# Kernel tuning notes

Hardware: AMD Instinct MI355X
Metric: run time of the kernel (lower is better)

Reference implementation:

```python
import jax, jax.numpy as jnp
import numpy as np

N, E = 20000, 320000
IN, OUT, MID, EC, L = 128, 128, 32, 32, 1
SQRT3 = 1.7320508075688772
EPS = 1e-5


def _xavier(key, fan_in, fan_out, shape=None):
    shape = shape if shape is not None else (fan_in, fan_out)
    std = (2.0 / (fan_in + fan_out)) ** 0.5
    return jax.random.normal(key, shape, dtype=jnp.float32) * std


def layer_norm(x, w, b):
    mu = x.mean(axis=-1, keepdims=True)
    var = ((x - mu) ** 2).mean(axis=-1, keepdims=True)
    return (x - mu) * jax.lax.rsqrt(var + EPS) * w + b


def equ_layer_norm(x, w, b, lmax):
    # x: [N, (lmax+1)^2, C]; per-l RMS norm over (m, channel); l=0 mean-centered + bias.
    segs = []
    for l in range(lmax + 1):
        f = x[:, l * l:(l + 1) * (l + 1), :]
        if l == 0:
            f = f - f.mean(axis=-1, keepdims=True)
        norm = jnp.mean(f * f, axis=(1, 2), keepdims=True)
        f = f * jax.lax.rsqrt(norm + EPS) * w[l]
        if l == 0:
            f = f + b
        segs.append(f)
    return jnp.concatenate(segs, axis=1)


def gate_3j(x, w, lmax, channel):
    # x: [N, (lmax+1)^2, C]; w: [C, C*(lmax+1)] (jax in,out layout)
    after = x[:, 0, :] @ w
    type0 = after[:, :channel]
    mult = jax.nn.sigmoid(after[:, channel:])  # [N, lmax*C]
    parts = [jax.nn.silu(type0)[:, None, :]]
    for l in range(1, lmax + 1):
        parts.append(x[:, l * l:(l + 1) * (l + 1), :] * mult[:, None, (l - 1) * channel:l * channel])
    return jnp.concatenate(parts, axis=1)


def setup_inputs() -> dict:
    key = jax.random.key(0)
    ks = jax.random.split(key, 24)
    inp = {
        'feats': jax.random.normal(ks[0], (N, IN), dtype=jnp.float32),
        'equ': jax.random.normal(ks[1], (N, (L + 1) ** 2, EC), dtype=jnp.float32),
        'points': jax.random.normal(ks[2], (N, 3), dtype=jnp.float32),
        'neighbors': jax.random.randint(ks[3], (2, E), 0, N, dtype=jnp.int64) if jax.config.jax_enable_x64 else jax.random.randint(ks[3], (2, E), 0, N, dtype=jnp.int32),
        # params (jax Linear layout: [in, out])
        'ln1_w': jnp.ones((IN,), jnp.float32), 'ln1_b': jnp.zeros((IN,), jnp.float32),
        'eqn1_w': jnp.ones((L + 1, EC), jnp.float32), 'eqn1_b': jnp.zeros((EC,), jnp.float32),
        'inv_fc_w': _xavier(ks[4], IN, MID), 'inv_fc_b': jnp.zeros((MID,), jnp.float32),
        'equ_fc_w': _xavier(ks[5], EC, MID),
        'fc_l0_w': _xavier(ks[6], 2 * MID, MID), 'fc_l0_b': jnp.zeros((MID,), jnp.float32),
        'equ_fc_2_w': _xavier(ks[7], MID, EC),
        'inv_fc_1_w': _xavier(ks[8], 3 * MID, OUT), 'inv_fc_1_b': jnp.zeros((OUT,), jnp.float32),
        'ffn_ln_w': jnp.ones((OUT,), jnp.float32), 'ffn_ln_b': jnp.zeros((OUT,), jnp.float32),
        'ffn_w1': _xavier(ks[9], OUT, OUT), 'ffn_b1': jnp.zeros((OUT,), jnp.float32),
        'ffn_w2': _xavier(ks[10], OUT, OUT), 'ffn_b2': jnp.zeros((OUT,), jnp.float32),
        'eqn2_w': jnp.ones((L + 1, EC), jnp.float32), 'eqn2_b': jnp.zeros((EC,), jnp.float32),
        'fe1_w': _xavier(ks[11], EC, MID),
        'gate_w': _xavier(ks[12], MID, MID * (L + 1)),
        'fe2_w': _xavier(ks[13], MID, EC),
    }
    return inp


def reference(feats, equ, points, neighbors, ln1_w, ln1_b, eqn1_w, eqn1_b,
              inv_fc_w, inv_fc_b, equ_fc_w, fc_l0_w, fc_l0_b, equ_fc_2_w,
              inv_fc_1_w, inv_fc_1_b, ffn_ln_w, ffn_ln_b, ffn_w1, ffn_b1,
              ffn_w2, ffn_b2, eqn2_w, eqn2_b, fe1_w, gate_w, fe2_w):
    n = feats.shape[0]
    feats = layer_norm(feats, ln1_w, ln1_b)
    equ = equ_layer_norm(equ, eqn1_w, eqn1_b, L)
    feats1 = feats @ inv_fc_w + inv_fc_b              # [N, MID]
    equ1 = equ @ equ_fc_w                              # [N, 4, MID]
    src, dst = neighbors[0], neighbors[1]
    s_equ, t_equ = equ1[src], equ1[dst]                # [E, 4, MID]
    s_feats, t_feats = feats1[src], feats1[dst]        # [E, MID]
    vec = points[src] - points[dst]                    # [E, 3]
    # e3nn spherical harmonics l=0..1, normalize=False, 'component': [1, sqrt(3)*v]
    sh = jnp.concatenate([jnp.ones((vec.shape[0], 1), vec.dtype), SQRT3 * vec], axis=1)  # [E, 4]
    dot1 = jnp.sum(s_equ * t_equ, axis=1)              # [E, MID]
    dot2 = jnp.sum(s_equ * sh[:, :, None], axis=1)     # [E, MID]
    equ_l0 = jax.nn.silu(jnp.concatenate([dot1, dot2], axis=1) @ fc_l0_w + fc_l0_b)
    equ_message = jnp.concatenate([equ_l0[:, None, :], s_equ[:, 1:, :]], axis=1)  # [E, 4, MID]
    equ_message = equ_message @ equ_fc_2_w             # [E, 4, EC]
    inv_message = jax.nn.silu(jnp.concatenate([s_feats, t_feats, equ_l0], axis=-1) @ inv_fc_1_w + inv_fc_1_b)  # [E, OUT]
    nb_cnt = (jnp.max(inv_message, axis=-1, keepdims=True) > 0.0).astype(feats.dtype)  # [E, 1]
    neighbors_new = jnp.ones((n, 1), feats.dtype).at[dst].add(nb_cnt)
    inv_new = jnp.zeros((n, OUT), feats.dtype).at[dst].add(inv_message) + feats  # shortcut1 = Identity
    inv_new = inv_new / neighbors_new
    equ_new = jnp.zeros((n, (L + 1) ** 2, EC), feats.dtype).at[dst].add(equ_message) + equ  # shortcut2 = Identity
    equ_new = equ_new / neighbors_new[:, :, None]
    # ffn_inv
    h = layer_norm(inv_new, ffn_ln_w, ffn_ln_b)
    h = jax.nn.relu(h @ ffn_w1 + ffn_b1) @ ffn_w2 + ffn_b2
    inv_new = h + inv_new
    # ffn_equ
    g = equ_layer_norm(equ_new, eqn2_w, eqn2_b, L) @ fe1_w
    g = gate_3j(g, gate_w, L, MID) @ fe2_w
    equ_new = g + equ_new
    return inv_new, equ_new
```

## Files before the change

kernel.cpp:

```cpp
#include <hip/hip_runtime.h>
#include <math.h>

#define EPS 1e-5f
#define SQRT3F 1.7320508075688772f

__device__ __forceinline__ float wsum64(float x) {
#pragma unroll
    for (int o = 32; o > 0; o >>= 1) x += __shfl_xor(x, o, 64);
    return x;
}
__device__ __forceinline__ float hsum32(float x) {
#pragma unroll
    for (int o = 16; o > 0; o >>= 1) x += __shfl_xor(x, o, 64);
    return x;
}
__device__ __forceinline__ float sigm(float x) { return 1.f / (1.f + __expf(-x)); }
__device__ __forceinline__ float siluf(float x) { return x * sigm(x); }

__global__ __launch_bounds__(256) void pre_and_hist(
    int N, int E, int nb_pre,
    const float* __restrict__ feats, const float* __restrict__ equ,
    const int* __restrict__ nbrs, const float* __restrict__ points,
    const float* __restrict__ ln1_w, const float* __restrict__ ln1_b,
    const float* __restrict__ eqn1_w, const float* __restrict__ eqn1_b,
    const float* __restrict__ inv_fc_w, const float* __restrict__ inv_fc_b,
    const float* __restrict__ equ_fc_w, const float* __restrict__ Winv,
    float* __restrict__ feats_ln, float* __restrict__ equ_ln,
    float* __restrict__ equ1t, float* __restrict__ PsP, float* __restrict__ PtP,
    float* __restrict__ points4, int* __restrict__ deg)
{
    if (blockIdx.x >= nb_pre) {
        int i = (blockIdx.x - nb_pre) * 256 + threadIdx.x;
        if (i < E) atomicAdd(&deg[nbrs[E + i]], 1);
        return;
    }

    __shared__ float fl_s[4][128];
    __shared__ float el_s[4][128];
    __shared__ float f1_s[4][32];
    const int w = threadIdx.x >> 6;
    const int lane = threadIdx.x & 63;
    const int n = blockIdx.x * 4 + w;
    const bool act = n < N;
    const int c = lane & 31;
    const int half = lane >> 5;

    if (act && lane == 0) {
        float4 p;
        p.x = points[n * 3 + 0]; p.y = points[n * 3 + 1];
        p.z = points[n * 3 + 2]; p.w = 0.f;
        *(float4*)&points4[n * 4] = p;
    }

    float x0 = 0.f, x1 = 0.f;
    if (act) { x0 = feats[n * 128 + lane]; x1 = feats[n * 128 + 64 + lane]; }
    float s  = wsum64(x0 + x1);
    float sq = wsum64(x0 * x0 + x1 * x1);
    float mu = s * (1.f / 128.f);
    float var = sq * (1.f / 128.f) - mu * mu;
    float rs = rsqrtf(var + EPS);
    float y0 = (x0 - mu) * rs * ln1_w[lane] + ln1_b[lane];
    float y1 = (x1 - mu) * rs * ln1_w[64 + lane] + ln1_b[64 + lane];
    if (act) { feats_ln[n * 128 + lane] = y0; feats_ln[n * 128 + 64 + lane] = y1; }
    fl_s[w][lane] = y0; fl_s[w][64 + lane] = y1;

    float a = 0.f, b = 0.f;
    if (act) { a = equ[n * 128 + lane]; b = equ[n * 128 + 64 + lane]; }
    float a0 = (half == 0) ? a : 0.f;
    float m0 = wsum64(a0) * (1.f / 32.f);
    float f0 = a0 - m0;
    float n0 = wsum64((half == 0) ? f0 * f0 : 0.f) * (1.f / 32.f);
    float rs0 = rsqrtf(n0 + EPS);
    float sq1 = ((half == 1) ? a * a : 0.f) + b * b;
    float n1 = wsum64(sq1) * (1.f / 96.f);
    float rs1 = rsqrtf(n1 + EPS);
    float w1c = eqn1_w[32 + c];
    float ea = (half == 0) ? (f0 * rs0 * eqn1_w[c] + eqn1_b[c]) : (a * rs1 * w1c);
    float eb = b * rs1 * w1c;
    if (act) { equ_ln[n * 128 + lane] = ea; equ_ln[n * 128 + 64 + lane] = eb; }
    el_s[w][lane] = ea; el_s[w][64 + lane] = eb;

    __syncthreads();

    {
        float acc = 0.f;
#pragma unroll 8
        for (int k = 0; k < 64; k++) {
            int kk = half * 64 + k;
            acc += fl_s[w][kk] * inv_fc_w[kk * 32 + c];
        }
        acc += __shfl_xor(acc, 32);
        if (half == 0) f1_s[w][c] = acc + inv_fc_b[c];
    }
    if (act) {
        float acc = 0.f, acc2 = 0.f;
#pragma unroll 8
        for (int k = 0; k < 32; k++) {
            float wv = equ_fc_w[k * 32 + c];
            acc  += el_s[w][half * 32 + k] * wv;
            acc2 += el_s[w][(half + 2) * 32 + k] * wv;
        }
        equ1t[n * 128 + c * 4 + half]     = acc;
        equ1t[n * 128 + c * 4 + half + 2] = acc2;
    }
    __syncthreads();
    if (!act) return;

    {
        const int jj = c;
        float4 aPs = {0.f, 0.f, 0.f, 0.f};
        float4 aPt = {0.f, 0.f, 0.f, 0.f};
#pragma unroll 4
        for (int k = 0; k < 16; k++) {
            int kk = half * 16 + k;
            float x = f1_s[w][kk];
            float4 w4 = *(const float4*)&Winv[kk * 128 + jj * 4];
            float4 v4 = *(const float4*)&Winv[(32 + kk) * 128 + jj * 4];
            aPs.x += x * w4.x; aPs.y += x * w4.y; aPs.z += x * w4.z; aPs.w += x * w4.w;
            aPt.x += x * v4.x; aPt.y += x * v4.y; aPt.z += x * v4.z; aPt.w += x * v4.w;
        }
        aPs.x += __shfl_xor(aPs.x, 32); aPs.y += __shfl_xor(aPs.y, 32);
        aPs.z += __shfl_xor(aPs.z, 32); aPs.w += __shfl_xor(aPs.w, 32);
        aPt.x += __shfl_xor(aPt.x, 32); aPt.y += __shfl_xor(aPt.y, 32);
        aPt.z += __shfl_xor(aPt.z, 32); aPt.w += __shfl_xor(aPt.w, 32);
        if (half == 0) {
            const float* ps = (const float*)&aPs;
            const float* pt = (const float*)&aPt;
#pragma unroll
            for (int i = 0; i < 4; i++) {
                int m = jj * 4 + i;
                PsP[n * 128 + (m & 31) * 4 + (m >> 5)] = ps[i];
                PtP[n * 128 + (m & 31) * 4 + (m >> 5)] = pt[i];
            }
        }
    }
}

__global__ __launch_bounds__(1024) void csr_scan(
    int N, const int* __restrict__ deg,
    int* __restrict__ row_start, int* __restrict__ cursor,
    int* __restrict__ bucket_start, int* __restrict__ bucket_cursor,
    const float* __restrict__ fe1, const float* __restrict__ fe2,
    const float* __restrict__ gate_w, const float* __restrict__ We2,
    float* __restrict__ fe1P, float* __restrict__ fe2P,
    float* __restrict__ gatePa, float* __restrict__ gatePb,
    float* __restrict__ We2P)
{
    __shared__ int part[1024];
    __shared__ int hist[64];
    const int t = threadIdx.x;

    if (t < 1024) {
        int g = t >> 7, r = t & 127, cc = r >> 2, i = r & 3;
        fe1P[t]   = fe1[(g * 4 + i) * 32 + cc];
        fe2P[t]   = fe2[(g * 4 + i) * 32 + cc];
        gatePa[t] = gate_w[(g * 4 + i) * 64 + cc];
        gatePb[t] = gate_w[(g * 4 + i) * 64 + 32 + cc];
        We2P[t]   = We2[(g * 4 + i) * 32 + cc];
    }

    if (t < 64) hist[t] = 0;
    __syncthreads();

    const int per = (N + 1023) / 1024;
    const int base = t * per;
    int s = 0;
    for (int i = 0; i < per; i++) {
        int idx = base + i;
        if (idx < N) {
            int d = deg[idx];
            s += d;
            atomicAdd(&hist[d < 63 ? d : 63], 1);
        }
    }
    part[t] = s;
    __syncthreads();
    for (int off = 1; off < 1024; off <<= 1) {
        int v = (t >= off) ? part[t - off] : 0;
        __syncthreads();
        part[t] += v;
        __syncthreads();
    }
    int run = (t > 0) ? part[t - 1] : 0;
    for (int i = 0; i < per; i++) {
        int idx = base + i;
        if (idx < N) { row_start[idx] = run; cursor[idx] = run; run += deg[idx]; }
    }
    if (t == 0) {
        int acc = 0;
        for (int b = 63; b >= 0; b--) {
            bucket_start[b] = acc;
            bucket_cursor[b] = acc;
            acc += hist[b];
        }
    }
}

__global__ __launch_bounds__(256) void scatter_all(
    int E, int N, int nbE,
    const int* __restrict__ nb, int* __restrict__ cursor, int* __restrict__ csr_src,
    const int* __restrict__ deg, int* __restrict__ bucket_cursor, int* __restrict__ perm)
{
    if (blockIdx.x < nbE) {
        int i = blockIdx.x * 256 + threadIdx.x;
        if (i < E) {
            int d = nb[E + i];
            int s = nb[i];
            int pos = atomicAdd(&cursor[d], 1);
            csr_src[pos] = s;
        }
    } else {
        int i = (blockIdx.x - nbE) * 256 + threadIdx.x;
        if (i < N) {
            int d = deg[i]; if (d > 63) d = 63;
            int pos = atomicAdd(&bucket_cursor[d], 1);
            perm[pos] = i;
        }
    }
}

__global__ __launch_bounds__(256) void edge_agg(
    int N,
    const int* __restrict__ perm,
    const int* __restrict__ row_start, const int* __restrict__ deg_arr,
    const int* __restrict__ csr_src,
    const float* __restrict__ points4, const float* __restrict__ equ1t,
    const float* __restrict__ PsP, const float* __restrict__ PtP,
    const float* __restrict__ feats_ln, const float* __restrict__ equ_ln,
    const float* __restrict__ Wl0g, const float* __restrict__ bl0g,
    const float* __restrict__ Winvg, const float* __restrict__ binvg,
    const float* __restrict__ We2P, const float* __restrict__ fe1P,
    const float* __restrict__ fe2P, const float* __restrict__ gatePa,
    const float* __restrict__ gatePb,
    const float* __restrict__ eqn2_w, const float* __restrict__ eqn2_b,
    float* __restrict__ out_inv, float* __restrict__ out_equ)
{
    __shared__ float WeP[32 * 128];
    __shared__ float Wl0P[16 * 128];
    __shared__ float BinvP[128];
    __shared__ float bl0s[32];
    __shared__ float scr[8][128];

    for (int idx = threadIdx.x; idx < 4096; idx += 256) {
        int k = idx >> 7, r = idx & 127, cc = r >> 2, j = r & 3;
        WeP[idx] = Winvg[(64 + k) * 128 + j * 32 + cc];
    }
    for (int idx = threadIdx.x; idx < 2048; idx += 256) {
        int g = idx >> 7, r = idx & 127, cc = r >> 2, i = r & 3;
        Wl0P[idx] = Wl0g[(g * 4 + i) * 32 + cc];
    }
    if (threadIdx.x < 128) BinvP[threadIdx.x] = binvg[(threadIdx.x & 3) * 32 + (threadIdx.x >> 2)];
    if (threadIdx.x < 32) bl0s[threadIdx.x] = bl0g[threadIdx.x];
    __syncthreads();

    const int grp = threadIdx.x >> 5;
    const int c = threadIdx.x & 31;
    const int halfsel = grp & 1;
    const int gid = blockIdx.x * 8 + grp;
    if (gid >= N) return;
    const int n = perm[gid];

    const int start = row_start[n];
    const int len = deg_arr[n];
    const float bl0c = bl0s[c];
    float4 te4 = *(const float4*)&equ1t[n * 128 + c * 4];
    float4 pt4 = *(const float4*)&PtP[n * 128 + c * 4];
    float4 pd4 = *(const float4*)&points4[n * 4];
    float4 base = *(const float4*)&BinvP[c * 4];
    base.x += pt4.x; base.y += pt4.y; base.z += pt4.z; base.w += pt4.w;

    float4 acc = {0.f, 0.f, 0.f, 0.f};
    float4 aer = {0.f, 0.f, 0.f, 0.f};
    int cnt = 0;
    int i = 0;

    for (; i + 2 <= len; i += 2) {
        const int s0 = csr_src[start + i];
        const int s1 = csr_src[start + i + 1];
        float4 a0 = *(const float4*)&equ1t[s0 * 128 + c * 4];
        float4 a1 = *(const float4*)&equ1t[s1 * 128 + c * 4];
        float4 p0 = *(const float4*)&PsP[s0 * 128 + c * 4];
        float4 p1 = *(const float4*)&PsP[s1 * 128 + c * 4];
        float4 q0 = *(const float4*)&points4[s0 * 4];
        float4 q1 = *(const float4*)&points4[s1 * 4];
        float dx0 = SQRT3F * (q0.x - pd4.x);
        float dy0 = SQRT3F * (q0.y - pd4.y);
        float dz0 = SQRT3F * (q0.z - pd4.z);
        float dx1 = SQRT3F * (q1.x - pd4.x);
        float dy1 = SQRT3F * (q1.y - pd4.y);
        float dz1 = SQRT3F * (q1.z - pd4.z);
        scr[grp][c]      = a0.x * te4.x + a0.y * te4.y + a0.z * te4.z + a0.w * te4.w;
        scr[grp][32 + c] = a0.x + a0.y * dx0 + a0.z * dy0 + a0.w * dz0;
        scr[grp][64 + c] = a1.x * te4.x + a1.y * te4.y + a1.z * te4.z + a1.w * te4.w;
        scr[grp][96 + c] = a1.x + a1.y * dx1 + a1.z * dy1 + a1.w * dz1;

        float e0acc = bl0c, e1acc = bl0c;
#pragma unroll
        for (int g = 0; g < 16; g++) {
            float4 w4 = *(const float4*)&Wl0P[g * 128 + c * 4];
            float4 d0 = *(const float4*)&scr[grp][g * 4];
            float4 d1 = *(const float4*)&scr[grp][64 + g * 4];
            e0acc += d0.x * w4.x + d0.y * w4.y + d0.z * w4.z + d0.w * w4.w;
            e1acc += d1.x * w4.x + d1.y * w4.y + d1.z * w4.z + d1.w * w4.w;
        }
        float el0_0 = siluf(e0acc);
        float el0_1 = siluf(e1acc);
        aer.x += el0_0 + el0_1;
        aer.y += a0.y + a1.y; aer.z += a0.z + a1.z; aer.w += a0.w + a1.w;
        scr[grp][c] = el0_0;
        scr[grp][32 + c] = el0_1;

        float4 m0 = base, m1 = base;
        m0.x += p0.x; m0.y += p0.y; m0.z += p0.z; m0.w += p0.w;
        m1.x += p1.x; m1.y += p1.y; m1.z += p1.z; m1.w += p1.w;
#pragma unroll
        for (int g = 0; g < 8; g++) {
            float4 x0 = *(const float4*)&scr[grp][g * 4];
            float4 x1 = *(const float4*)&scr[grp][32 + g * 4];
            const float* xp0 = (const float*)&x0;
            const float* xp1 = (const float*)&x1;
#pragma unroll
            for (int t = 0; t < 4; t++) {
                float4 w4 = *(const float4*)&WeP[(g * 4 + t) * 128 + c * 4];
                float v0 = xp0[t], v1 = xp1[t];
                m0.x += v0 * w4.x; m0.y += v0 * w4.y; m0.z += v0 * w4.z; m0.w += v0 * w4.w;
                m1.x += v1 * w4.x; m1.y += v1 * w4.y; m1.z += v1 * w4.z; m1.w += v1 * w4.w;
            }
        }
        m0.x = siluf(m0.x); m0.y = siluf(m0.y); m0.z = siluf(m0.z); m0.w = siluf(m0.w);
        m1.x = siluf(m1.x); m1.y = siluf(m1.y); m1.z = siluf(m1.z); m1.w = siluf(m1.w);
        acc.x += m0.x + m1.x; acc.y += m0.y + m1.y;
        acc.z += m0.z + m1.z; acc.w += m0.w + m1.w;
        float mx0 = fmaxf(fmaxf(m0.x, m0.y), fmaxf(m0.z, m0.w));
        float mx1 = fmaxf(fmaxf(m1.x, m1.y), fmaxf(m1.z, m1.w));
        unsigned long long b0 = __ballot(mx0 > 0.f);
        unsigned long long b1 = __ballot(mx1 > 0.f);
        cnt += ((unsigned int)(b0 >> (halfsel * 32)) != 0u);
        cnt += ((unsigned int)(b1 >> (halfsel * 32)) != 0u);
    }
    for (; i < len; i++) {
        const int s0 = csr_src[start + i];
        float4 a0 = *(const float4*)&equ1t[s0 * 128 + c * 4];
        float4 p0 = *(const float4*)&PsP[s0 * 128 + c * 4];
        float4 q0 = *(const float4*)&points4[s0 * 4];
        float dx0 = SQRT3F * (q0.x - pd4.x);
        float dy0 = SQRT3F * (q0.y - pd4.y);
        float dz0 = SQRT3F * (q0.z - pd4.z);
        scr[grp][c]      = a0.x * te4.x + a0.y * te4.y + a0.z * te4.z + a0.w * te4.w;
        scr[grp][32 + c] = a0.x + a0.y * dx0 + a0.z * dy0 + a0.w * dz0;
        float e0acc = bl0c;
#pragma unroll
        for (int g = 0; g < 16; g++) {
            float4 w4 = *(const float4*)&Wl0P[g * 128 + c * 4];
            float4 d0 = *(const float4*)&scr[grp][g * 4];
            e0acc += d0.x * w4.x + d0.y * w4.y + d0.z * w4.z + d0.w * w4.w;
        }
        float el0_0 = siluf(e0acc);
        aer.x += el0_0; aer.y += a0.y; aer.z += a0.z; aer.w += a0.w;
        scr[grp][c] = el0_0;
        float4 m0 = base;
        m0.x += p0.x; m0.y += p0.y; m0.z += p0.z; m0.w += p0.w;
#pragma unroll
        for (int g = 0; g < 8; g++) {
            float4 x0 = *(const float4*)&scr[grp][g * 4];
            const float* xp0 = (const float*)&x0;
#pragma unroll
            for (int t = 0; t < 4; t++) {
                float4 w4 = *(const float4*)&WeP[(g * 4 + t) * 128 + c * 4];
                float v0 = xp0[t];
                m0.x += v0 * w4.x; m0.y += v0 * w4.y; m0.z += v0 * w4.z; m0.w += v0 * w4.w;
            }
        }
        m0.x = siluf(m0.x); m0.y = siluf(m0.y); m0.z = siluf(m0.z); m0.w = siluf(m0.w);
        acc.x += m0.x; acc.y += m0.y; acc.z += m0.z; acc.w += m0.w;
        float mx0 = fmaxf(fmaxf(m0.x, m0.y), fmaxf(m0.z, m0.w));
        unsigned long long b0 = __ballot(mx0 > 0.f);
        cnt += ((unsigned int)(b0 >> (halfsel * 32)) != 0u);
    }

    const float inv_nbn = 1.f / (1.f + (float)cnt);
    out_inv[n * 128 + c]      = (acc.x + feats_ln[n * 128 + c])      * inv_nbn;
    out_inv[n * 128 + 32 + c] = (acc.y + feats_ln[n * 128 + 32 + c]) * inv_nbn;
    out_inv[n * 128 + 64 + c] = (acc.z + feats_ln[n * 128 + 64 + c]) * inv_nbn;
    out_inv[n * 128 + 96 + c] = (acc.w + feats_ln[n * 128 + 96 + c]) * inv_nbn;

    *(float4*)&scr[grp][c * 4] = aer;
    float4 eo = {0.f, 0.f, 0.f, 0.f};
#pragma unroll
    for (int g = 0; g < 8; g++) {
        float4 w4 = *(const float4*)&We2P[g * 128 + c * 4];
        const float* wp = (const float*)&w4;
#pragma unroll
        for (int t = 0; t < 4; t++) {
            float4 a4 = *(const float4*)&scr[grp][(g * 4 + t) * 4];
            float wv = wp[t];
            eo.x += a4.x * wv; eo.y += a4.y * wv; eo.z += a4.z * wv; eo.w += a4.w * wv;
        }
    }
    float4 en;
    en.x = (eo.x + equ_ln[n * 128 + c])      * inv_nbn;
    en.y = (eo.y + equ_ln[n * 128 + 32 + c]) * inv_nbn;
    en.z = (eo.z + equ_ln[n * 128 + 64 + c]) * inv_nbn;
    en.w = (eo.w + equ_ln[n * 128 + 96 + c]) * inv_nbn;

    float m0e = hsum32(en.x) * (1.f / 32.f);
    float f0 = en.x - m0e;
    float n0 = hsum32(f0 * f0) * (1.f / 32.f);
    float rs0 = rsqrtf(n0 + EPS);
    float n1 = hsum32(en.y * en.y + en.z * en.z + en.w * en.w) * (1.f / 96.f);
    float rs1 = rsqrtf(n1 + EPS);
    float w1c = eqn2_w[32 + c];
    float4 ev;
    ev.x = f0 * rs0 * eqn2_w[c] + eqn2_b[c];
    ev.y = en.y * rs1 * w1c;
    ev.z = en.z * rs1 * w1c;
    ev.w = en.w * rs1 * w1c;
    *(float4*)&scr[grp][c * 4] = ev;

    float4 g4 = {0.f, 0.f, 0.f, 0.f};
#pragma unroll
    for (int g = 0; g < 8; g++) {
        float4 w4 = *(const float4*)&fe1P[g * 128 + c * 4];
        const float* wp = (const float*)&w4;
#pragma unroll
        for (int t = 0; t < 4; t++) {
            float4 a4 = *(const float4*)&scr[grp][(g * 4 + t) * 4];
            float wv = wp[t];
            g4.x += a4.x * wv; g4.y += a4.y * wv; g4.z += a4.z * wv; g4.w += a4.w * wv;
        }
    }
    scr[grp][c] = g4.x;

    float aftA = 0.f, aftB = 0.f;
#pragma unroll
    for (int g = 0; g < 8; g++) {
        float4 x4 = *(const float4*)&scr[grp][g * 4];
        float4 wa4 = *(const float4*)&gatePa[g * 128 + c * 4];
        float4 wb4 = *(const float4*)&gatePb[g * 128 + c * 4];
        aftA += x4.x * wa4.x + x4.y * wa4.y + x4.z * wa4.z + x4.w * wa4.w;
        aftB += x4.x * wb4.x + x4.y * wb4.y + x4.z * wb4.z + x4.w * wb4.w;
    }
    float mult = sigm(aftB);
    float4 G;
    G.x = siluf(aftA);
    G.y = g4.y * mult; G.z = g4.z * mult; G.w = g4.w * mult;
    *(float4*)&scr[grp][c * 4] = G;

    float4 oo = {0.f, 0.f, 0.f, 0.f};
#pragma unroll
    for (int g = 0; g < 8; g++) {
        float4 w4 = *(const float4*)&fe2P[g * 128 + c * 4];
        const float* wp = (const float*)&w4;
#pragma unroll
        for (int t = 0; t < 4; t++) {
            float4 a4 = *(const float4*)&scr[grp][(g * 4 + t) * 4];
            float wv = wp[t];
            oo.x += a4.x * wv; oo.y += a4.y * wv; oo.z += a4.z * wv; oo.w += a4.w * wv;
        }
    }
    out_equ[n * 128 + c]      = oo.x + en.x;
    out_equ[n * 128 + 32 + c] = oo.y + en.y;
    out_equ[n * 128 + 64 + c] = oo.z + en.z;
    out_equ[n * 128 + 96 + c] = oo.w + en.w;
}

__global__ __launch_bounds__(256) void node_post(
    int N,
    const float* __restrict__ ffn_ln_w, const float* __restrict__ ffn_ln_b,
    const float* __restrict__ W1g, const float* __restrict__ b1g,
    const float* __restrict__ W2g, const float* __restrict__ b2g,
    float* __restrict__ io_inv)
{
    __shared__ float ht[128 * 36];
    const int grp = threadIdx.x >> 5;
    const int c = threadIdx.x & 31;

    for (int q = 0; q < 4; q++) {
        const int nd = grp * 4 + q;
        const int n = blockIdx.x * 32 + nd;
        if (n >= N) break;
        float ip0 = io_inv[n * 128 + c];
        float ip1 = io_inv[n * 128 + 32 + c];
        float ip2 = io_inv[n * 128 + 64 + c];
        float ip3 = io_inv[n * 128 + 96 + c];
        float sm = hsum32(ip0 + ip1 + ip2 + ip3) * (1.f / 128.f);
        float sv = hsum32(ip0 * ip0 + ip1 * ip1 + ip2 * ip2 + ip3 * ip3) * (1.f / 128.f) - sm * sm;
        float rsv = rsqrtf(sv + EPS);
        ht[c * 36 + nd]         = (ip0 - sm) * rsv * ffn_ln_w[c]      + ffn_ln_b[c];
        ht[(32 + c) * 36 + nd]  = (ip1 - sm) * rsv * ffn_ln_w[32 + c] + ffn_ln_b[32 + c];
        ht[(64 + c) * 36 + nd]  = (ip2 - sm) * rsv * ffn_ln_w[64 + c] + ffn_ln_b[64 + c];
        ht[(96 + c) * 36 + nd]  = (ip3 - sm) * rsv * ffn_ln_w[96 + c] + ffn_ln_b[96 + c];
    }

    const int wid = threadIdx.x >> 6;
    const int half = (threadIdx.x >> 5) & 1;
    const int ndbase = wid * 8;
    const int nbase = blockIdx.x * 32 + ndbase;

    float4 acc8[8];
#pragma unroll
    for (int j = 0; j < 8; j++) acc8[j] = make_float4(0.f, 0.f, 0.f, 0.f);
    for (int k = 0; k < 64; k++) {
        const int kk = half * 64 + k;
        float4 w4 = *(const float4*)&W1g[kk * 128 + c * 4];
        float4 xA = *(const float4*)&ht[kk * 36 + ndbase];
        float4 xB = *(const float4*)&ht[kk * 36 + ndbase + 4];
        const float* xa = (const float*)&xA;
        const float* xb = (const float*)&xB;
#pragma unroll
        for (int j = 0; j < 4; j++) {
            float v = xa[j];
            acc8[j].x += v * w4.x; acc8[j].y += v * w4.y; acc8[j].z += v * w4.z; acc8[j].w += v * w4.w;
            float u = xb[j];
            acc8[4 + j].x += u * w4.x; acc8[4 + j].y += u * w4.y; acc8[4 + j].z += u * w4.z; acc8[4 + j].w += u * w4.w;
        }
    }
#pragma unroll
    for (int j = 0; j < 8; j++) {
        acc8[j].x += __shfl_xor(acc8[j].x, 32); acc8[j].y += __shfl_xor(acc8[j].y, 32);
        acc8[j].z += __shfl_xor(acc8[j].z, 32); acc8[j].w += __shfl_xor(acc8[j].w, 32);
    }
    if (half == 0) {
        float4 b4 = *(const float4*)&b1g[c * 4];
#pragma unroll
        for (int j = 0; j < 8; j++) {
            ht[(4 * c + 0) * 36 + ndbase + j] = fmaxf(acc8[j].x + b4.x, 0.f);
            ht[(4 * c + 1) * 36 + ndbase + j] = fmaxf(acc8[j].y + b4.y, 0.f);
            ht[(4 * c + 2) * 36 + ndbase + j] = fmaxf(acc8[j].z + b4.z, 0.f);
            ht[(4 * c + 3) * 36 + ndbase + j] = fmaxf(acc8[j].w + b4.w, 0.f);
        }
    }
#pragma unroll
    for (int j = 0; j < 8; j++) acc8[j] = make_float4(0.f, 0.f, 0.f, 0.f);
    for (int k = 0; k < 64; k++) {
        const int kk = half * 64 + k;
        float4 w4 = *(const float4*)&W2g[kk * 128 + c * 4];
        float4 xA = *(const float4*)&ht[kk * 36 + ndbase];
        float4 xB = *(const float4*)&ht[kk * 36 + ndbase + 4];
        const float* xa = (const float*)&xA;
        const float* xb = (const float*)&xB;
#pragma unroll
        for (int j = 0; j < 4; j++) {
            float v = xa[j];
            acc8[j].x += v * w4.x; acc8[j].y += v * w4.y; acc8[j].z += v * w4.z; acc8[j].w += v * w4.w;
            float u = xb[j];
            acc8[4 + j].x += u * w4.x; acc8[4 + j].y += u * w4.y; acc8[4 + j].z += u * w4.z; acc8[4 + j].w += u * w4.w;
        }
    }
#pragma unroll
    for (int j = 0; j < 8; j++) {
        acc8[j].x += __shfl_xor(acc8[j].x, 32); acc8[j].y += __shfl_xor(acc8[j].y, 32);
        acc8[j].z += __shfl_xor(acc8[j].z, 32); acc8[j].w += __shfl_xor(acc8[j].w, 32);
    }
    if (half == 0) {
        float4 b4 = *(const float4*)&b2g[c * 4];
#pragma unroll
        for (int j = 0; j < 8; j++) {
            const int n = nbase + j;
            if (n < N) {
                float4 ipre = *(const float4*)&io_inv[n * 128 + c * 4];
                float4 o;
                o.x = acc8[j].x + b4.x + ipre.x;
                o.y = acc8[j].y + b4.y + ipre.y;
                o.z = acc8[j].z + b4.z + ipre.z;
                o.w = acc8[j].w + b4.w + ipre.w;
                *(float4*)&io_inv[n * 128 + c * 4] = o;
            }
        }
    }
}

extern "C" void kernel_launch(void* const* d_in, const int* in_sizes, int n_in,
                              void* d_out, int out_size, void* d_ws, size_t ws_size,
                              hipStream_t stream)
{
    const float* feats     = (const float*)d_in[0];
    const float* equ       = (const float*)d_in[1];
    const float* points    = (const float*)d_in[2];
    const int*   neighbors = (const int*)d_in[3];
    const float* ln1_w     = (const float*)d_in[4];
    const float* ln1_b     = (const float*)d_in[5];
    const float* eqn1_w    = (const float*)d_in[6];
    const float* eqn1_b    = (const float*)d_in[7];
    const float* inv_fc_w  = (const float*)d_in[8];
    const float* inv_fc_b  = (const float*)d_in[9];
    const float* equ_fc_w  = (const float*)d_in[10];
    const float* fc_l0_w   = (const float*)d_in[11];
    const float* fc_l0_b   = (const float*)d_in[12];
    const float* equ_fc_2_w= (const float*)d_in[13];
    const float* inv_fc_1_w= (const float*)d_in[14];
    const float* inv_fc_1_b= (const float*)d_in[15];
    const float* ffn_ln_w  = (const float*)d_in[16];
    const float* ffn_ln_b  = (const float*)d_in[17];
    const float* ffn_w1    = (const float*)d_in[18];
    const float* ffn_b1    = (const float*)d_in[19];
    const float* ffn_w2    = (const float*)d_in[20];
    const float* ffn_b2    = (const float*)d_in[21];
    const float* eqn2_w    = (const float*)d_in[22];
    const float* eqn2_b    = (const float*)d_in[23];
    const float* fe1_w     = (const float*)d_in[24];
    const float* gate_w    = (const float*)d_in[25];
    const float* fe2_w     = (const float*)d_in[26];

    const int N = in_sizes[0] / 128;
    const int E = in_sizes[3] / 2;

    float* ws = (float*)d_ws;
    float* feats_ln = ws;
    float* equ_ln   = feats_ln + (size_t)N * 128;
    float* equ1t    = equ_ln   + (size_t)N * 128;
    float* PsP      = equ1t    + (size_t)N * 128;
    float* PtP      = PsP      + (size_t)N * 128;
    float* points4  = PtP      + (size_t)N * 128;
    float* fe1P     = points4  + (size_t)N * 4;
    float* fe2P     = fe1P + 1024;
    float* gatePa   = fe2P + 1024;
    float* gatePb   = gatePa + 1024;
    float* We2P     = gatePb + 1024;
    int* deg        = (int*)(We2P + 1024);
    int* row_start  = deg + N;
    int* cursor     = row_start + N;
    int* bucket_start  = cursor + N;
    int* bucket_cursor = bucket_start + 64;
    int* perm       = bucket_cursor + 64;
    int* csr_src    = perm + N;

    hipMemsetAsync(deg, 0, (size_t)N * sizeof(int), stream);

    const int nb_pre = (N + 3) / 4;
    const int nb_hist = (E + 255) / 256;
    pre_and_hist<<<nb_pre + nb_hist, 256, 0, stream>>>(
        N, E, nb_pre, feats, equ, neighbors, points,
        ln1_w, ln1_b, eqn1_w, eqn1_b,
        inv_fc_w, inv_fc_b, equ_fc_w, inv_fc_1_w,
        feats_ln, equ_ln, equ1t, PsP, PtP, points4, deg);

    csr_scan<<<1, 1024, 0, stream>>>(
        N, deg, row_start, cursor, bucket_start, bucket_cursor,
        fe1_w, fe2_w, gate_w, equ_fc_2_w,
        fe1P, fe2P, gatePa, gatePb, We2P);

    const int nbE = (E + 255) / 256;
    const int nbN = (N + 255) / 256;
    scatter_all<<<nbE + nbN, 256, 0, stream>>>(
        E, N, nbE, neighbors, cursor, csr_src, deg, bucket_cursor, perm);

    float* out_inv = (float*)d_out;
    float* out_equ = out_inv + (size_t)N * 128;

    edge_agg<<<(N + 7) / 8, 256, 0, stream>>>(
        N, perm, row_start, deg, csr_src,
        points4, equ1t, PsP, PtP, feats_ln, equ_ln,
        fc_l0_w, fc_l0_b, inv_fc_1_w, inv_fc_1_b,
        We2P, fe1P, fe2P, gatePa, gatePb, eqn2_w, eqn2_b,
        out_inv, out_equ);

    node_post<<<(N + 31) / 32, 256, 0, stream>>>(
        N, ffn_ln_w, ffn_ln_b, ffn_w1, ffn_b1, ffn_w2, ffn_b2,
        out_inv);
}
```

Before: 476.7 us.

## Fuse node FFN (layernorm + MLP) into edge aggregation kernel epilogue

Removes the separate node_post kernel and computes the inverse-feature layer norm and two-layer FFN inside edge_agg, keeping the aggregated node features in shared memory instead of writing and rereading them from global memory. The perm array is padded with -1 so every thread reaches the block-wide barrier, and only two waves per block run the 128x128 matmuls with weights read from global memory. This saves a launch and a global round-trip, but adds shared memory (less occupancy), a barrier that makes each block wait for its slowest-degree node, and a serial FFN tail using only a quarter of the threads.

```diff
diff --git a/kernel.cpp b/kernel.cpp
--- a/kernel.cpp
+++ b/kernel.cpp
@@ -137,9 +137,10 @@
 }
 
 __global__ __launch_bounds__(1024) void csr_scan(
-    int N, const int* __restrict__ deg,
+    int N, int nblk, const int* __restrict__ deg,
     int* __restrict__ row_start, int* __restrict__ cursor,
     int* __restrict__ bucket_start, int* __restrict__ bucket_cursor,
+    int* __restrict__ perm,
     const float* __restrict__ fe1, const float* __restrict__ fe2,
     const float* __restrict__ gate_w, const float* __restrict__ We2,
     float* __restrict__ fe1P, float* __restrict__ fe2P,
@@ -157,6 +158,9 @@
         gatePa[t] = gate_w[(g * 4 + i) * 64 + cc];
         gatePb[t] = gate_w[(g * 4 + i) * 64 + 32 + cc];
         We2P[t]   = We2[(g * 4 + i) * 32 + cc];
+    }
+    if (t == 1) {
+        for (int j = N; j < nblk * 8; j++) perm[j] = -1;
     }
 
     if (t < 64) hist[t] = 0;
@@ -233,6 +237,9 @@
     const float* __restrict__ fe2P, const float* __restrict__ gatePa,
     const float* __restrict__ gatePb,
     const float* __restrict__ eqn2_w, const float* __restrict__ eqn2_b,
+    const float* __restrict__ ffn_ln_w, const float* __restrict__ ffn_ln_b,
+    const float* __restrict__ W1g, const float* __restrict__ b1g,
+    const float* __restrict__ W2g, const float* __restrict__ b2g,
     float* __restrict__ out_inv, float* __restrict__ out_equ)
 {
     __shared__ float WeP[32 * 128];
@@ -240,6 +247,9 @@
     __shared__ float BinvP[128];
     __shared__ float bl0s[32];
     __shared__ float scr[8][128];
+    __shared__ float invs[8][128];
+    __shared__ float htp[128 * 9];
+    __shared__ int   nid[8];
 
     for (int idx = threadIdx.x; idx < 4096; idx += 256) {
         int k = idx >> 7, r = idx & 127, cc = r >> 2, j = r & 3;
@@ -257,314 +267,312 @@
     const int c = threadIdx.x & 31;
     const int halfsel = grp & 1;
     const int gid = blockIdx.x * 8 + grp;
-    if (gid >= N) return;
     const int n = perm[gid];
-
-    const int start = row_start[n];
-    const int len = deg_arr[n];
-    const float bl0c = bl0s[c];
-    float4 te4 = *(const float4*)&equ1t[n * 128 + c * 4];
-    float4 pt4 = *(const float4*)&PtP[n * 128 + c * 4];
-    float4 pd4 = *(const float4*)&points4[n * 4];
-    float4 base = *(const float4*)&BinvP[c * 4];
-    base.x += pt4.x; base.y += pt4.y; base.z += pt4.z; base.w += pt4.w;
-
-    float4 acc = {0.f, 0.f, 0.f, 0.f};
-    float4 aer = {0.f, 0.f, 0.f, 0.f};
-    int cnt = 0;
-    int i = 0;
-
-    for (; i + 2 <= len; i += 2) {
-        const int s0 = csr_src[start + i];
-        const int s1 = csr_src[start + i + 1];
-        float4 a0 = *(const float4*)&equ1t[s0 * 128 + c * 4];
-        float4 a1 = *(const float4*)&equ1t[s1 * 128 + c * 4];
-        float4 p0 = *(const float4*)&PsP[s0 * 128 + c * 4];
-        float4 p1 = *(const float4*)&PsP[s1 * 128 + c * 4];
-        float4 q0 = *(const float4*)&points4[s0 * 4];
-        float4 q1 = *(const float4*)&points4[s1 * 4];
-        float dx0 = SQRT3F * (q0.x - pd4.x);
-        float dy0 = SQRT3F * (q0.y - pd4.y);
-        float dz0 = SQRT3F * (q0.z - pd4.z);
-        float dx1 = SQRT3F * (q1.x - pd4.x);
-        float dy1 = SQRT3F * (q1.y - pd4.y);
-        float dz1 = SQRT3F * (q1.z - pd4.z);
-        scr[grp][c]      = a0.x * te4.x + a0.y * te4.y + a0.z * te4.z + a0.w * te4.w;
-        scr[grp][32 + c] = a0.x + a0.y * dx0 + a0.z * dy0 + a0.w * dz0;
-        scr[grp][64 + c] = a1.x * te4.x + a1.y * te4.y + a1.z * te4.z + a1.w * te4.w;
-        scr[grp][96 + c] = a1.x + a1.y * dx1 + a1.z * dy1 + a1.w * dz1;
-
-        float e0acc = bl0c, e1acc = bl0c;
-#pragma unroll
-        for (int g = 0; g < 16; g++) {
-            float4 w4 = *(const float4*)&Wl0P[g * 128 + c * 4];
-            float4 d0 = *(const float4*)&scr[grp][g * 4];
-            float4 d1 = *(const float4*)&scr[grp][64 + g * 4];
-            e0acc += d0.x * w4.x + d0.y * w4.y + d0.z * w4.z + d0.w * w4.w;
-            e1acc += d1.x * w4.x + d1.y * w4.y + d1.z * w4.z + d1.w * w4.w;
-        }
-        float el0_0 = siluf(e0acc);
-        float el0_1 = siluf(e1acc);
-        aer.x += el0_0 + el0_1;
-        aer.y += a0.y + a1.y; aer.z += a0.z + a1.z; aer.w += a0.w + a1.w;
-        scr[grp][c] = el0_0;
-        scr[grp][32 + c] = el0_1;
-
-        float4 m0 = base, m1 = base;
-        m0.x += p0.x; m0.y += p0.y; m0.z += p0.z; m0.w += p0.w;
-        m1.x += p1.x; m1.y += p1.y; m1.z += p1.z; m1.w += p1.w;
+    if (c == 0) nid[grp] = n;
+    const bool active = (n >= 0);
+
+    if (active) {
+        const int start = row_start[n];
+        const int len = deg_arr[n];
+        const float bl0c = bl0s[c];
+        float4 te4 = *(const float4*)&equ1t[n * 128 + c * 4];
+        float4 pt4 = *(const float4*)&PtP[n * 128 + c * 4];
+        float4 pd4 = *(const float4*)&points4[n * 4];
+        float4 base = *(const float4*)&BinvP[c * 4];
+        base.x += pt4.x; base.y += pt4.y; base.z += pt4.z; base.w += pt4.w;
+
+        float4 acc = {0.f, 0.f, 0.f, 0.f};
+        float4 aer = {0.f, 0.f, 0.f, 0.f};
+        int cnt = 0;
+        int i = 0;
+
+        for (; i + 2 <= len; i += 2) {
+            const int s0 = csr_src[start + i];
+            const int s1 = csr_src[start + i + 1];
+            float4 a0 = *(const float4*)&equ1t[s0 * 128 + c * 4];
+            float4 a1 = *(const float4*)&equ1t[s1 * 128 + c * 4];
+            float4 p0 = *(const float4*)&PsP[s0 * 128 + c * 4];
+            float4 p1 = *(const float4*)&PsP[s1 * 128 + c * 4];
+            float4 q0 = *(const float4*)&points4[s0 * 4];
+            float4 q1 = *(const float4*)&points4[s1 * 4];
+            float dx0 = SQRT3F * (q0.x - pd4.x);
+            float dy0 = SQRT3F * (q0.y - pd4.y);
+            float dz0 = SQRT3F * (q0.z - pd4.z);
+            float dx1 = SQRT3F * (q1.x - pd4.x);
+            float dy1 = SQRT3F * (q1.y - pd4.y);
+            float dz1 = SQRT3F * (q1.z - pd4.z);
+            scr[grp][c]      = a0.x * te4.x + a0.y * te4.y + a0.z * te4.z + a0.w * te4.w;
+            scr[grp][32 + c] = a0.x + a0.y * dx0 + a0.z * dy0 + a0.w * dz0;
+            scr[grp][64 + c] = a1.x * te4.x + a1.y * te4.y + a1.z * te4.z + a1.w * te4.w;
+            scr[grp][96 + c] = a1.x + a1.y * dx1 + a1.z * dy1 + a1.w * dz1;
+
+            float e0acc = bl0c, e1acc = bl0c;
+#pragma unroll
+            for (int g = 0; g < 16; g++) {
+                float4 w4 = *(const float4*)&Wl0P[g * 128 + c * 4];
+                float4 d0 = *(const float4*)&scr[grp][g * 4];
+                float4 d1 = *(const float4*)&scr[grp][64 + g * 4];
+                e0acc += d0.x * w4.x + d0.y * w4.y + d0.z * w4.z + d0.w * w4.w;
+                e1acc += d1.x * w4.x + d1.y * w4.y + d1.z * w4.z + d1.w * w4.w;
+            }
+            float el0_0 = siluf(e0acc);
+            float el0_1 = siluf(e1acc);
+            aer.x += el0_0 + el0_1;
+            aer.y += a0.y + a1.y; aer.z += a0.z + a1.z; aer.w += a0.w + a1.w;
+            scr[grp][c] = el0_0;
+            scr[grp][32 + c] = el0_1;
+
+            float4 m0 = base, m1 = base;
+            m0.x += p0.x; m0.y += p0.y; m0.z += p0.z; m0.w += p0.w;
+            m1.x += p1.x; m1.y += p1.y; m1.z += p1.z; m1.w += p1.w;
+#pragma unroll
+            for (int g = 0; g < 8; g++) {
+                float4 x0 = *(const float4*)&scr[grp][g * 4];
+                float4 x1 = *(const float4*)&scr[grp][32 + g * 4];
+                const float* xp0 = (const float*)&x0;
+                const float* xp1 = (const float*)&x1;
+#pragma unroll
+                for (int t = 0; t < 4; t++) {
+                    float4 w4 = *(const float4*)&WeP[(g * 4 + t) * 128 + c * 4];
+                    float v0 = xp0[t], v1 = xp1[t];
+                    m0.x += v0 * w4.x; m0.y += v0 * w4.y; m0.z += v0 * w4.z; m0.w += v0 * w4.w;
+                    m1.x += v1 * w4.x; m1.y += v1 * w4.y; m1.z += v1 * w4.z; m1.w += v1 * w4.w;
+                }
+            }
+            m0.x = siluf(m0.x); m0.y = siluf(m0.y); m0.z = siluf(m0.z); m0.w = siluf(m0.w);
+            m1.x = siluf(m1.x); m1.y = siluf(m1.y); m1.z = siluf(m1.z); m1.w = siluf(m1.w);
+            acc.x += m0.x + m1.x; acc.y += m0.y + m1.y;
+            acc.z += m0.z + m1.z; acc.w += m0.w + m1.w;
+            float mx0 = fmaxf(fmaxf(m0.x, m0.y), fmaxf(m0.z, m0.w));
+            float mx1 = fmaxf(fmaxf(m1.x, m1.y), fmaxf(m1.z, m1.w));
+            unsigned long long b0 = __ballot(mx0 > 0.f);
+            unsigned long long b1 = __ballot(mx1 > 0.f);
+            cnt += ((unsigned int)(b0 >> (halfsel * 32)) != 0u);
+            cnt += ((unsigned int)(b1 >> (halfsel * 32)) != 0u);
+        }
+        for (; i < len; i++) {
+            const int s0 = csr_src[start + i];
+            float4 a0 = *(const float4*)&equ1t[s0 * 128 + c * 4];
+            float4 p0 = *(const float4*)&PsP[s0 * 128 + c * 4];
+            float4 q0 = *(const float4*)&points4[s0 * 4];
+            float dx0 = SQRT3F * (q0.x - pd4.x);
+            float dy0 = SQRT3F * (q0.y - pd4.y);
+            float dz0 = SQRT3F * (q0.z - pd4.z);
+            scr[grp][c]      = a0.x * te4.x + a0.y * te4.y + a0.z * te4.z + a0.w * te4.w;
+            scr[grp][32 + c] = a0.x + a0.y * dx0 + a0.z * dy0 + a0.w * dz0;
+            float e0acc = bl0c;
+#pragma unroll
+            for (int g = 0; g < 16; g++) {
+                float4 w4 = *(const float4*)&Wl0P[g * 128 + c * 4];
+                float4 d0 = *(const float4*)&scr[grp][g * 4];
+                e0acc += d0.x * w4.x + d0.y * w4.y + d0.z * w4.z + d0.w * w4.w;
+            }
+            float el0_0 = siluf(e0acc);
+            aer.x += el0_0; aer.y += a0.y; aer.z += a0.z; aer.w += a0.w;
+            scr[grp][c] = el0_0;
+            float4 m0 = base;
+            m0.x += p0.x; m0.y += p0.y; m0.z += p0.z; m0.w += p0.w;
+#pragma unroll
+            for (int g = 0; g < 8; g++) {
+                float4 x0 = *(const float4*)&scr[grp][g * 4];
+                const float* xp0 = (const float*)&x0;
+#pragma unroll
+                for (int t = 0; t < 4; t++) {
+                    float4 w4 = *(const float4*)&WeP[(g * 4 + t) * 128 + c * 4];
+                    float v0 = xp0[t];
+                    m0.x += v0 * w4.x; m0.y += v0 * w4.y; m0.z += v0 * w4.z; m0.w += v0 * w4.w;
+                }
+            }
+            m0.x = siluf(m0.x); m0.y = siluf(m0.y); m0.z = siluf(m0.z); m0.w = siluf(m0.w);
+            acc.x += m0.x; acc.y += m0.y; acc.z += m0.z; acc.w += m0.w;
+            float mx0 = fmaxf(fmaxf(m0.x, m0.y), fmaxf(m0.z, m0.w));
+            unsigned long long b0 = __ballot(mx0 > 0.f);
+            cnt += ((unsigned int)(b0 >> (halfsel * 32)) != 0u);
+        }
+
+        const float inv_nbn = 1.f / (1.f + (float)cnt);
+        float4 im;
+        im.x = (acc.x + feats_ln[n * 128 + c])      * inv_nbn;
+        im.y = (acc.y + feats_ln[n * 128 + 32 + c]) * inv_nbn;
+        im.z = (acc.z + feats_ln[n * 128 + 64 + c]) * inv_nbn;
+        im.w = (acc.w + feats_ln[n * 128 + 96 + c]) * inv_nbn;
+        invs[grp][c]      = im.x;
+        invs[grp][32 + c] = im.y;
+        invs[grp][64 + c] = im.z;
+        invs[grp][96 + c] = im.w;
+        float sm = hsum32(im.x + im.y + im.z + im.w) * (1.f / 128.f);
+        float sv = hsum32(im.x * im.x + im.y * im.y + im.z * im.z + im.w * im.w)
+                   * (1.f / 128.f) - sm * sm;
+        float rsv = rsqrtf(sv + EPS);
+        htp[c * 9 + grp]        = (im.x - sm) * rsv * ffn_ln_w[c]      + ffn_ln_b[c];
+        htp[(32 + c) * 9 + grp] = (im.y - sm) * rsv * ffn_ln_w[32 + c] + ffn_ln_b[32 + c];
+        htp[(64 + c) * 9 + grp] = (im.z - sm) * rsv * ffn_ln_w[64 + c] + ffn_ln_b[64 + c];
+        htp[(96 + c) * 9 + grp] = (im.w - sm) * rsv * ffn_ln_w[96 + c] + ffn_ln_b[96 + c];
+
+        *(float4*)&scr[grp][c * 4] = aer;
+        float4 eo = {0.f, 0.f, 0.f, 0.f};
 #pragma unroll
         for (int g = 0; g < 8; g++) {
-            float4 x0 = *(const float4*)&scr[grp][g * 4];
-            float4 x1 = *(const float4*)&scr[grp][32 + g * 4];
-            const float* xp0 = (const float*)&x0;
-            const float* xp1 = (const float*)&x1;
+            float4 w4 = *(const float4*)&We2P[g * 128 + c * 4];
+            const float* wp = (const float*)&w4;
 #pragma unroll
             for (int t = 0; t < 4; t++) {
-                float4 w4 = *(const float4*)&WeP[(g * 4 + t) * 128 + c * 4];
-                float v0 = xp0[t], v1 = xp1[t];
-                m0.x += v0 * w4.x; m0.y += v0 * w4.y; m0.z += v0 * w4.z; m0.w += v0 * w4.w;
-                m1.x += v1 * w4.x; m1.y += v1 * w4.y; m1.z += v1 * w4.z; m1.w += v1 * w4.w;
-            }
-        }
-        m0.x = siluf(m0.x); m0.y = siluf(m0.y); m0.z = siluf(m0.z); m0.w = siluf(m0.w);
-        m1.x = siluf(m1.x); m1.y = siluf(m1.y); m1.z = siluf(m1.z); m1.w = siluf(m1.w);
-        acc.x += m0.x + m1.x; acc.y += m0.y + m1.y;
-        acc.z += m0.z + m1.z; acc.w += m0.w + m1.w;
-        float mx0 = fmaxf(fmaxf(m0.x, m0.y), fmaxf(m0.z, m0.w));
-        float mx1 = fmaxf(fmaxf(m1.x, m1.y), fmaxf(m1.z, m1.w));
-        unsigned long long b0 = __ballot(mx0 > 0.f);
-        unsigned long long b1 = __ballot(mx1 > 0.f);
-        cnt += ((unsigned int)(b0 >> (halfsel * 32)) != 0u);
-        cnt += ((unsigned int)(b1 >> (halfsel * 32)) != 0u);
-    }
-    for (; i < len; i++) {
-        const int s0 = csr_src[start + i];
-        float4 a0 = *(const float4*)&equ1t[s0 * 128 + c * 4];
-        float4 p0 = *(const float4*)&PsP[s0 * 128 + c * 4];
-        float4 q0 = *(const float4*)&points4[s0 * 4];
-        float dx0 = SQRT3F * (q0.x - pd4.x);
-        float dy0 = SQRT3F * (q0.y - pd4.y);
-        float dz0 = SQRT3F * (q0.z - pd4.z);
-        scr[grp][c]      = a0.x * te4.x + a0.y * te4.y + a0.z * te4.z + a0.w * te4.w;
-        scr[grp][32 + c] = a0.x + a0.y * dx0 + a0.z * dy0 + a0.w * dz0;
-        float e0acc = bl0c;
-#pragma unroll
-        for (int g = 0; g < 16; g++) {
-            float4 w4 = *(const float4*)&Wl0P[g * 128 + c * 4];
-            float4 d0 = *(const float4*)&scr[grp][g * 4];
-            e0acc += d0.x * w4.x + d0.y * w4.y + d0.z * w4.z + d0.w * w4.w;
-        }
-        float el0_0 = siluf(e0acc);
-        aer.x += el0_0; aer.y += a0.y; aer.z += a0.z; aer.w += a0.w;
-        scr[grp][c] = el0_0;
-        float4 m0 = base;
-        m0.x += p0.x; m0.y += p0.y; m0.z += p0.z; m0.w += p0.w;
+                float4 a4 = *(const float4*)&scr[grp][(g * 4 + t) * 4];
+                float wv = wp[t];
+                eo.x += a4.x * wv; eo.y += a4.y * wv; eo.z += a4.z * wv; eo.w += a4.w * wv;
+            }
+        }
+        float4 en;
+        en.x = (eo.x + equ_ln[n * 128 + c])      * inv_nbn;
+        en.y = (eo.y + equ_ln[n * 128 + 32 + c]) * inv_nbn;
+        en.z = (eo.z + equ_ln[n * 128 + 64 + c]) * inv_nbn;
+        en.w = (eo.w + equ_ln[n * 128 + 96 + c]) * inv_nbn;
+
+        float m0e = hsum32(en.x) * (1.f / 32.f);
+        float f0 = en.x - m0e;
+        float n0 = hsum32(f0 * f0) * (1.f / 32.f);
+        float rs0 = rsqrtf(n0 + EPS);
+        float n1 = hsum32(en.y * en.y + en.z * en.z + en.w * en.w) * (1.f / 96.f);
+        float rs1 = rsqrtf(n1 + EPS);
+        float w1c = eqn2_w[32 + c];
+        float4 ev;
+        ev.x = f0 * rs0 * eqn2_w[c] + eqn2_b[c];
+        ev.y = en.y * rs1 * w1c;
+        ev.z = en.z * rs1 * w1c;
+        ev.w = en.w * rs1 * w1c;
+        *(float4*)&scr[grp][c * 4] = ev;
+
+        float4 g4 = {0.f, 0.f, 0.f, 0.f};
 #pragma unroll
         for (int g = 0; g < 8; g++) {
-            float4 x0 = *(const float4*)&scr[grp][g * 4];
-            const float* xp0 = (const float*)&x0;
+            float4 w4 = *(const float4*)&fe1P[g * 128 + c * 4];
+            const float* wp = (const float*)&w4;
 #pragma unroll
             for (int t = 0; t < 4; t++) {
-                float4 w4 = *(const float4*)&WeP[(g * 4 + t) * 128 + c * 4];
-                float v0 = xp0[t];
-                m0.x += v0 * w4.x; m0.y += v0 * w4.y; m0.z += v0 * w4.z; m0.w += v0 * w4.w;
-            }
-        }
-        m0.x = siluf(m0.x); m0.y = siluf(m0.y); m0.z = siluf(m0.z); m0.w = siluf(m0.w);
-        acc.x += m0.x; acc.y += m0.y; acc.z += m0.z; acc.w += m0.w;
-        float mx0 = fmaxf(fmaxf(m0.x, m0.y), fmaxf(m0.z, m0.w));
-        unsigned long long b0 = __ballot(mx0 > 0.f);
-        cnt += ((unsigned int)(b0 >> (halfsel * 32)) != 0u);
-    }
-
-    const float inv_nbn = 1.f / (1.f + (float)cnt);
-    out_inv[n * 128 + c]      = (acc.x + feats_ln[n * 128 + c])      * inv_nbn;
-    out_inv[n * 128 + 32 + c] = (acc.y + feats_ln[n * 128 + 32 + c]) * inv_nbn;
-    out_inv[n * 128 + 64 + c] = (acc.z + feats_ln[n * 128 + 64 + c]) * inv_nbn;
-    out_inv[n * 128 + 96 + c] = (acc.w + feats_ln[n * 128 + 96 + c]) * inv_nbn;
-
-    *(float4*)&scr[grp][c * 4] = aer;
-    float4 eo = {0.f, 0.f, 0.f, 0.f};
-#pragma unroll
-    for (int g = 0; g < 8; g++) {
-        float4 w4 = *(const float4*)&We2P[g * 128 + c * 4];
-        const float* wp = (const float*)&w4;
-#pragma unroll
-        for (int t = 0; t < 4; t++) {
-            float4 a4 = *(const float4*)&scr[grp][(g * 4 + t) * 4];
-            float wv = wp[t];
-            eo.x += a4.x * wv; eo.y += a4.y * wv; eo.z += a4.z * wv; eo.w += a4.w * wv;
-        }
-    }
-    float4 en;
-    en.x = (eo.x + equ_ln[n * 128 + c])      * inv_nbn;
-    en.y = (eo.y + equ_ln[n * 128 + 32 + c]) * inv_nbn;
-    en.z = (eo.z + equ_ln[n * 128 + 64 + c]) * inv_nbn;
-    en.w = (eo.w + equ_ln[n * 128 + 96 + c]) * inv_nbn;
-
-    float m0e = hsum32(en.x) * (1.f / 32.f);
-    float f0 = en.x - m0e;
-    float n0 = hsum32(f0 * f0) * (1.f / 32.f);
-    float rs0 = rsqrtf(n0 + EPS);
-    float n1 = hsum32(en.y * en.y + en.z * en.z + en.w * en.w) * (1.f / 96.f);
-    float rs1 = rsqrtf(n1 + EPS);
-    float w1c = eqn2_w[32 + c];
-    float4 ev;
-    ev.x = f0 * rs0 * eqn2_w[c] + eqn2_b[c];
-    ev.y = en.y * rs1 * w1c;
-    ev.z = en.z * rs1 * w1c;
-    ev.w = en.w * rs1 * w1c;
-    *(float4*)&scr[grp][c * 4] = ev;
-
-    float4 g4 = {0.f, 0.f, 0.f, 0.f};
-#pragma unroll
-    for (int g = 0; g < 8; g++) {
-        float4 w4 = *(const float4*)&fe1P[g * 128 + c * 4];
-        const float* wp = (const float*)&w4;
-#pragma unroll
-        for (int t = 0; t < 4; t++) {
-            float4 a4 = *(const float4*)&scr[grp][(g * 4 + t) * 4];
-            float wv = wp[t];
-            g4.x += a4.x * wv; g4.y += a4.y * wv; g4.z += a4.z * wv; g4.w += a4.w * wv;
-        }
-    }
-    scr[grp][c] = g4.x;
-
-    float aftA = 0.f, aftB = 0.f;
-#pragma unroll
-    for (int g = 0; g < 8; g++) {
-        float4 x4 = *(const float4*)&scr[grp][g * 4];
-        float4 wa4 = *(const float4*)&gatePa[g * 128 + c * 4];
-        float4 wb4 = *(const float4*)&gatePb[g * 128 + c * 4];
-        aftA += x4.x * wa4.x + x4.y * wa4.y + x4.z * wa4.z + x4.w * wa4.w;
-        aftB += x4.x * wb4.x + x4.y * wb4.y + x4.z * wb4.z + x4.w * wb4.w;
-    }
-    float mult = sigm(aftB);
-    float4 G;
-    G.x = siluf(aftA);
-    G.y = g4.y * mult; G.z = g4.z * mult; G.w = g4.w * mult;
-    *(float4*)&scr[grp][c * 4] = G;
-
-    float4 oo = {0.f, 0.f, 0.f, 0.f};
-#pragma unroll
-    for (int g = 0; g < 8; g++) {
-        float4 w4 = *(const float4*)&fe2P[g * 128 + c * 4];
-        const float* wp = (const float*)&w4;
-#pragma unroll
-        for (int t = 0; t < 4; t++) {
-            float4 a4 = *(const float4*)&scr[grp][(g * 4 + t) * 4];
-            float wv = wp[t];
-            oo.x += a4.x * wv; oo.y += a4.y * wv; oo.z += a4.z * wv; oo.w += a4.w * wv;
-        }
-    }
-    out_equ[n * 128 + c]      = oo.x + en.x;
-    out_equ[n * 128 + 32 + c] = oo.y + en.y;
-    out_equ[n * 128 + 64 + c] = oo.z + en.z;
-    out_equ[n * 128 + 96 + c] = oo.w + en.w;
-}
-
-__global__ __launch_bounds__(256) void node_post(
-    int N,
-    const float* __restrict__ ffn_ln_w, const float* __restrict__ ffn_ln_b,
-    const float* __restrict__ W1g, const float* __restrict__ b1g,
-    const float* __restrict__ W2g, const float* __restrict__ b2g,
-    float* __restrict__ io_inv)
-{
-    __shared__ float ht[128 * 36];
-    const int grp = threadIdx.x >> 5;
-    const int c = threadIdx.x & 31;
-
-    for (int q = 0; q < 4; q++) {
-        const int nd = grp * 4 + q;
-        const int n = blockIdx.x * 32 + nd;
-        if (n >= N) break;
-        float ip0 = io_inv[n * 128 + c];
-        float ip1 = io_inv[n * 128 + 32 + c];
-        float ip2 = io_inv[n * 128 + 64 + c];
-        float ip3 = io_inv[n * 128 + 96 + c];
-        float sm = hsum32(ip0 + ip1 + ip2 + ip3) * (1.f / 128.f);
-        float sv = hsum32(ip0 * ip0 + ip1 * ip1 + ip2 * ip2 + ip3 * ip3) * (1.f / 128.f) - sm * sm;
-        float rsv = rsqrtf(sv + EPS);
-        ht[c * 36 + nd]         = (ip0 - sm) * rsv * ffn_ln_w[c]      + ffn_ln_b[c];
-        ht[(32 + c) * 36 + nd]  = (ip1 - sm) * rsv * ffn_ln_w[32 + c] + ffn_ln_b[32 + c];
-        ht[(64 + c) * 36 + nd]  = (ip2 - sm) * rsv * ffn_ln_w[64 + c] + ffn_ln_b[64 + c];
-        ht[(96 + c) * 36 + nd]  = (ip3 - sm) * rsv * ffn_ln_w[96 + c] + ffn_ln_b[96 + c];
-    }
-
-    const int wid = threadIdx.x >> 6;
-    const int half = (threadIdx.x >> 5) & 1;
-    const int ndbase = wid * 8;
-    const int nbase = blockIdx.x * 32 + ndbase;
-
-    float4 acc8[8];
-#pragma unroll
-    for (int j = 0; j < 8; j++) acc8[j] = make_float4(0.f, 0.f, 0.f, 0.f);
-    for (int k = 0; k < 64; k++) {
-        const int kk = half * 64 + k;
-        float4 w4 = *(const float4*)&W1g[kk * 128 + c * 4];
-        float4 xA = *(const float4*)&ht[kk * 36 + ndbase];
-        float4 xB = *(const float4*)&ht[kk * 36 + ndbase + 4];
-        const float* xa = (const float*)&xA;
-        const float* xb = (const float*)&xB;
-#pragma unroll
-        for (int j = 0; j < 4; j++) {
-            float v = xa[j];
-            acc8[j].x += v * w4.x; acc8[j].y += v * w4.y; acc8[j].z += v * w4.z; acc8[j].w += v * w4.w;
-            float u = xb[j];
-            acc8[4 + j].x += u * w4.x; acc8[4 + j].y += u * w4.y; acc8[4 + j].z += u * w4.z; acc8[4 + j].w += u * w4.w;
-        }
-    }
-#pragma unroll
-    for (int j = 0; j < 8; j++) {
-        acc8[j].x += __shfl_xor(acc8[j].x, 32); acc8[j].y += __shfl_xor(acc8[j].y, 32);
-        acc8[j].z += __shfl_xor(acc8[j].z, 32); acc8[j].w += __shfl_xor(acc8[j].w, 32);
-    }
-    if (half == 0) {
-        float4 b4 = *(const float4*)&b1g[c * 4];
-#pragma unroll
-        for (int j = 0; j < 8; j++) {
-            ht[(4 * c + 0) * 36 + ndbase + j] = fmaxf(acc8[j].x + b4.x, 0.f);
-            ht[(4 * c + 1) * 36 + ndbase + j] = fmaxf(acc8[j].y + b4.y, 0.f);
-            ht[(4 * c + 2) * 36 + ndbase + j] = fmaxf(acc8[j].z + b4.z, 0.f);
-            ht[(4 * c + 3) * 36 + ndbase + j] = fmaxf(acc8[j].w + b4.w, 0.f);
-        }
-    }
-#pragma unroll
-    for (int j = 0; j < 8; j++) acc8[j] = make_float4(0.f, 0.f, 0.f, 0.f);
-    for (int k = 0; k < 64; k++) {
-        const int kk = half * 64 + k;
-        float4 w4 = *(const float4*)&W2g[kk * 128 + c * 4];
-        float4 xA = *(const float4*)&ht[kk * 36 + ndbase];
-        float4 xB = *(const float4*)&ht[kk * 36 + ndbase + 4];
-        const float* xa = (const float*)&xA;
-        const float* xb = (const float*)&xB;
-#pragma unroll
-        for (int j = 0; j < 4; j++) {
-            float v = xa[j];
-            acc8[j].x += v * w4.x; acc8[j].y += v * w4.y; acc8[j].z += v * w4.z; acc8[j].w += v * w4.w;
-            float u = xb[j];
-            acc8[4 + j].x += u * w4.x; acc8[4 + j].y += u * w4.y; acc8[4 + j].z += u * w4.z; acc8[4 + j].w += u * w4.w;
-        }
-    }
-#pragma unroll
-    for (int j = 0; j < 8; j++) {
-        acc8[j].x += __shfl_xor(acc8[j].x, 32); acc8[j].y += __shfl_xor(acc8[j].y, 32);
-        acc8[j].z += __shfl_xor(acc8[j].z, 32); acc8[j].w += __shfl_xor(acc8[j].w, 32);
-    }
-    if (half == 0) {
-        float4 b4 = *(const float4*)&b2g[c * 4];
-#pragma unroll
-        for (int j = 0; j < 8; j++) {
-            const int n = nbase + j;
-            if (n < N) {
-                float4 ipre = *(const float4*)&io_inv[n * 128 + c * 4];
-                float4 o;
-                o.x = acc8[j].x + b4.x + ipre.x;
-                o.y = acc8[j].y + b4.y + ipre.y;
-                o.z = acc8[j].z + b4.z + ipre.z;
-                o.w = acc8[j].w + b4.w + ipre.w;
-                *(float4*)&io_inv[n * 128 + c * 4] = o;
+                float4 a4 = *(const float4*)&scr[grp][(g * 4 + t) * 4];
+                float wv = wp[t];
+                g4.x += a4.x * wv; g4.y += a4.y * wv; g4.z += a4.z * wv; g4.w += a4.w * wv;
+            }
+        }
+        scr[grp][c] = g4.x;
+
+        float aftA = 0.f, aftB = 0.f;
+#pragma unroll
+        for (int g = 0; g < 8; g++) {
+            float4 x4 = *(const float4*)&scr[grp][g * 4];
+            float4 wa4 = *(const float4*)&gatePa[g * 128 + c * 4];
+            float4 wb4 = *(const float4*)&gatePb[g * 128 + c * 4];
+            aftA += x4.x * wa4.x + x4.y * wa4.y + x4.z * wa4.z + x4.w * wa4.w;
+            aftB += x4.x * wb4.x + x4.y * wb4.y + x4.z * wb4.z + x4.w * wb4.w;
+        }
+        float mult = sigm(aftB);
+        float4 G;
+        G.x = siluf(aftA);
+        G.y = g4.y * mult; G.z = g4.z * mult; G.w = g4.w * mult;
+        *(float4*)&scr[grp][c * 4] = G;
+
+        float4 oo = {0.f, 0.f, 0.f, 0.f};
+#pragma unroll
+        for (int g = 0; g < 8; g++) {
+            float4 w4 = *(const float4*)&fe2P[g * 128 + c * 4];
+            const float* wp = (const float*)&w4;
+#pragma unroll
+            for (int t = 0; t < 4; t++) {
+                float4 a4 = *(const float4*)&scr[grp][(g * 4 + t) * 4];
+                float wv = wp[t];
+                oo.x += a4.x * wv; oo.y += a4.y * wv; oo.z += a4.z * wv; oo.w += a4.w * wv;
+            }
+        }
+        out_equ[n * 128 + c]      = oo.x + en.x;
+        out_equ[n * 128 + 32 + c] = oo.y + en.y;
+        out_equ[n * 128 + 64 + c] = oo.z + en.z;
+        out_equ[n * 128 + 96 + c] = oo.w + en.w;
+    }
+
+    __syncthreads();
+    {
+        const int wid = threadIdx.x >> 6;
+        if (wid < 2) {
+            const int half = (threadIdx.x >> 5) & 1;
+            const int nb0 = wid * 4;
+            float4 A0 = {0,0,0,0}, A1 = {0,0,0,0}, A2 = {0,0,0,0}, A3 = {0,0,0,0};
+            for (int k = 0; k < 64; k++) {
+                const int kk = half * 64 + k;
+                float4 w4 = *(const float4*)&W1g[kk * 128 + c * 4];
+                float x0 = htp[kk * 9 + nb0 + 0];
+                float x1 = htp[kk * 9 + nb0 + 1];
+                float x2 = htp[kk * 9 + nb0 + 2];
+                float x3 = htp[kk * 9 + nb0 + 3];
+                A0.x += x0 * w4.x; A0.y += x0 * w4.y; A0.z += x0 * w4.z; A0.w += x0 * w4.w;
+                A1.x += x1 * w4.x; A1.y += x1 * w4.y; A1.z += x1 * w4.z; A1.w += x1 * w4.w;
+                A2.x += x2 * w4.x; A2.y += x2 * w4.y; A2.z += x2 * w4.z; A2.w += x2 * w4.w;
+                A3.x += x3 * w4.x; A3.y += x3 * w4.y; A3.z += x3 * w4.z; A3.w += x3 * w4.w;
+            }
+            A0.x += __shfl_xor(A0.x, 32); A0.y += __shfl_xor(A0.y, 32);
+            A0.z += __shfl_xor(A0.z, 32); A0.w += __shfl_xor(A0.w, 32);
+            A1.x += __shfl_xor(A1.x, 32); A1.y += __shfl_xor(A1.y, 32);
+            A1.z += __shfl_xor(A1.z, 32); A1.w += __shfl_xor(A1.w, 32);
+            A2.x += __shfl_xor(A2.x, 32); A2.y += __shfl_xor(A2.y, 32);
+            A2.z += __shfl_xor(A2.z, 32); A2.w += __shfl_xor(A2.w, 32);
+            A3.x += __shfl_xor(A3.x, 32); A3.y += __shfl_xor(A3.y, 32);
+            A3.z += __shfl_xor(A3.z, 32); A3.w += __shfl_xor(A3.w, 32);
+            if (half == 0) {
+                float4 b4 = *(const float4*)&b1g[c * 4];
+                htp[(4 * c + 0) * 9 + nb0 + 0] = fmaxf(A0.x + b4.x, 0.f);
+                htp[(4 * c + 1) * 9 + nb0 + 0] = fmaxf(A0.y + b4.y, 0.f);
+                htp[(4 * c + 2) * 9 + nb0 + 0] = fmaxf(A0.z + b4.z, 0.f);
+                htp[(4 * c + 3) * 9 + nb0 + 0] = fmaxf(A0.w + b4.w, 0.f);
+                htp[(4 * c + 0) * 9 + nb0 + 1] = fmaxf(A1.x + b4.x, 0.f);
+                htp[(4 * c + 1) * 9 + nb0 + 1] = fmaxf(A1.y + b4.y, 0.f);
+                htp[(4 * c + 2) * 9 + nb0 + 1] = fmaxf(A1.z + b4.z, 0.f);
+                htp[(4 * c + 3) * 9 + nb0 + 1] = fmaxf(A1.w + b4.w, 0.f);
+                htp[(4 * c + 0) * 9 + nb0 + 2] = fmaxf(A2.x + b4.x, 0.f);
+                htp[(4 * c + 1) * 9 + nb0 + 2] = fmaxf(A2.y + b4.y, 0.f);
+                htp[(4 * c + 2) * 9 + nb0 + 2] = fmaxf(A2.z + b4.z, 0.f);
+                htp[(4 * c + 3) * 9 + nb0 + 2] = fmaxf(A2.w + b4.w, 0.f);
+                htp[(4 * c + 0) * 9 + nb0 + 3] = fmaxf(A3.x + b4.x, 0.f);
+                htp[(4 * c + 1) * 9 + nb0 + 3] = fmaxf(A3.y + b4.y, 0.f);
+                htp[(4 * c + 2) * 9 + nb0 + 3] = fmaxf(A3.z + b4.z, 0.f);
+                htp[(4 * c + 3) * 9 + nb0 + 3] = fmaxf(A3.w + b4.w, 0.f);
+            }
+            A0 = make_float4(0,0,0,0); A1 = make_float4(0,0,0,0);
+            A2 = make_float4(0,0,0,0); A3 = make_float4(0,0,0,0);
+            for (int k = 0; k < 64; k++) {
+                const int kk = half * 64 + k;
+                float4 w4 = *(const float4*)&W2g[kk * 128 + c * 4];
+                float x0 = htp[kk * 9 + nb0 + 0];
+                float x1 = htp[kk * 9 + nb0 + 1];
+                float x2 = htp[kk * 9 + nb0 + 2];
+                float x3 = htp[kk * 9 + nb0 + 3];
+                A0.x += x0 * w4.x; A0.y += x0 * w4.y; A0.z += x0 * w4.z; A0.w += x0 * w4.w;
+                A1.x += x1 * w4.x; A1.y += x1 * w4.y; A1.z += x1 * w4.z; A1.w += x1 * w4.w;
+                A2.x += x2 * w4.x; A2.y += x2 * w4.y; A2.z += x2 * w4.z; A2.w += x2 * w4.w;
+                A3.x += x3 * w4.x; A3.y += x3 * w4.y; A3.z += x3 * w4.z; A3.w += x3 * w4.w;
+            }
+            A0.x += __shfl_xor(A0.x, 32); A0.y += __shfl_xor(A0.y, 32);
+            A0.z += __shfl_xor(A0.z, 32); A0.w += __shfl_xor(A0.w, 32);
+            A1.x += __shfl_xor(A1.x, 32); A1.y += __shfl_xor(A1.y, 32);
+            A1.z += __shfl_xor(A1.z, 32); A1.w += __shfl_xor(A1.w, 32);
+            A2.x += __shfl_xor(A2.x, 32); A2.y += __shfl_xor(A2.y, 32);
+            A2.z += __shfl_xor(A2.z, 32); A2.w += __shfl_xor(A2.w, 32);
+            A3.x += __shfl_xor(A3.x, 32); A3.y += __shfl_xor(A3.y, 32);
+            A3.z += __shfl_xor(A3.z, 32); A3.w += __shfl_xor(A3.w, 32);
+            if (half == 0) {
+                float4 b4 = *(const float4*)&b2g[c * 4];
+                float4 A[4] = {A0, A1, A2, A3};
+#pragma unroll
+                for (int j = 0; j < 4; j++) {
+                    const int nn = nid[nb0 + j];
+                    if (nn >= 0) {
+                        float4 r4 = *(const float4*)&invs[nb0 + j][c * 4];
+                        float4 o;
+                        o.x = A[j].x + b4.x + r4.x;
+                        o.y = A[j].y + b4.y + r4.y;
+                        o.z = A[j].z + b4.z + r4.z;
+                        o.w = A[j].w + b4.w + r4.w;
+                        *(float4*)&out_inv[(size_t)nn * 128 + c * 4] = o;
+                    }
+                }
             }
         }
     }
@@ -604,6 +612,7 @@
 
     const int N = in_sizes[0] / 128;
     const int E = in_sizes[3] / 2;
+    const int nblk = (N + 7) / 8;
 
     float* ws = (float*)d_ws;
     float* feats_ln = ws;
@@ -623,7 +632,7 @@
     int* bucket_start  = cursor + N;
     int* bucket_cursor = bucket_start + 64;
     int* perm       = bucket_cursor + 64;
-    int* csr_src    = perm + N;
+    int* csr_src    = perm + (size_t)nblk * 8;
 
     hipMemsetAsync(deg, 0, (size_t)N * sizeof(int), stream);
 
@@ -636,7 +645,7 @@
         feats_ln, equ_ln, equ1t, PsP, PtP, points4, deg);
 
     csr_scan<<<1, 1024, 0, stream>>>(
-        N, deg, row_start, cursor, bucket_start, bucket_cursor,
+        N, nblk, deg, row_start, cursor, bucket_start, bucket_cursor, perm,
         fe1_w, fe2_w, gate_w, equ_fc_2_w,
         fe1P, fe2P, gatePa, gatePb, We2P);
 
@@ -648,14 +657,11 @@
     float* out_inv = (float*)d_out;
     float* out_equ = out_inv + (size_t)N * 128;
 
-    edge_agg<<<(N + 7) / 8, 256, 0, stream>>>(
+    edge_agg<<<nblk, 256, 0, stream>>>(
         N, perm, row_start, deg, csr_src,
         points4, equ1t, PsP, PtP, feats_ln, equ_ln,
         fc_l0_w, fc_l0_b, inv_fc_1_w, inv_fc_1_b,
         We2P, fe1P, fe2P, gatePa, gatePb, eqn2_w, eqn2_b,
+        ffn_ln_w, ffn_ln_b, ffn_w1, ffn_b1, ffn_w2, ffn_b2,
         out_inv, out_equ);
-
-    node_post<<<(N + 31) / 32, 256, 0, stream>>>(
-        N, ffn_ln_w, ffn_ln_b, ffn_w1, ffn_b1, ffn_w2, ffn_b2,
-        out_inv);
 }
```

After: 705.0 us. +47.9%, slower.
